# Kernel tuning notes

Measured on AMD Instinct MI355X. Metric: run time of the kernel, lower is better.

The kernel has to match this reference:

```python
import jax, jax.numpy as jnp
import numpy as np

H, B, F, D1, D21, D22, C = 10, 16384, 4, 2048, 2048, 2048, 2
OBS_X, OBS_Y, RADIUS = 40.0, 15.0, 6.0


def setup_inputs() -> dict:
    key = jax.random.key(0)
    ks = jax.random.split(key, 12)
    s = 0.02  # weight scale
    return {
        'x':   jax.random.normal(ks[0], (B, F), jnp.float32),
        'W1':  jax.random.normal(ks[1], (H, F, D1), jnp.float32) * s,
        'b1':  jnp.zeros((H, D1), jnp.float32),
        'W21': jax.random.normal(ks[2], (H, D1, D21), jnp.float32) * s,
        'b21': jnp.zeros((H, D21), jnp.float32),
        'W22': jax.random.normal(ks[3], (H, D1, D22), jnp.float32) * s,
        'b22': jnp.zeros((H, D22), jnp.float32),
        'W31': jax.random.normal(ks[4], (H, D21, C), jnp.float32) * s,
        'b31': jnp.zeros((H, C), jnp.float32),
        'W32': jax.random.normal(ks[5], (H, D22, C), jnp.float32) * s,
        'b32': jnp.zeros((H, C), jnp.float32),
        'wt':  jnp.ones((H,), jnp.float32),
        'mean': jax.random.normal(ks[6], (F,), jnp.float32),
        'std':  jnp.ones((F,), jnp.float32),
        'sgn': 1,
        'itr': 0,
    }


def reference(x, W1, b1, W21, b21, W22, b22, W31, b31, W32, b32, wt, mean, std, sgn, itr):
    # x: [B,F]; un-normalized state x0 = x*std + mean
    x0 = x * std + mean

    # --- 10-head small-MLP ensemble (batched over heads via einsum) ---
    h1  = jax.nn.relu(jnp.einsum('bf,hfd->hbd', x, W1) + b1[:, None, :])      # [H,B,D1]
    x21 = jax.nn.relu(jnp.einsum('hbd,hde->hbe', h1, W21) + b21[:, None, :])  # [H,B,D21]
    x22 = jax.nn.relu(jnp.einsum('hbd,hde->hbe', h1, W22) + b22[:, None, :])  # [H,B,D22]
    x31 = jnp.einsum('hbe,hec->hbc', x21, W31) + b31[:, None, :]              # [H,B,C] nominal control
    x32 = 4.0 * jax.nn.sigmoid(jnp.einsum('hbe,hec->hbc', x22, W32) + b32[:, None, :])  # [H,B,C] CBF params

    # --- dCBF constraint (shared across heads; depends only on x0) ---
    px, py, theta, v = x0[:, 0], x0[:, 1], x0[:, 2], x0[:, 3]
    dx, dy = px - OBS_X, py - OBS_Y
    st, ct = jnp.sin(theta), jnp.cos(theta)
    barrier = dx * dx + dy * dy - RADIUS * RADIUS                 # [B]
    barrier_dot = 2.0 * dx * v * ct + 2.0 * dy * v * st          # [B]
    Lf2b = 2.0 * v * v                                            # [B]
    LgLfbu1 = -2.0 * dx * v * st + 2.0 * dy * v * ct
    LgLfbu2 = 2.0 * dx * ct + 2.0 * dy * st
    G = jnp.stack([-LgLfbu1, -LgLfbu2], axis=-1)                  # [B,C]

    # sgn == 1 -> same branch for every head (i==0 or sgn==1)
    h_rhs = Lf2b + (x32[..., 0] + x32[..., 1]) * barrier_dot + x32[..., 0] * x32[..., 1] * barrier  # [H,B]

    # --- batched QP: min 0.5 u'u - x31'u  s.t. G u <= h  (Q = I) ---
    # closed-form single-constraint active set: u = x31 - relu(G.x31 - h)/||G||^2 * G
    Gu = jnp.einsum('bc,hbc->hb', G, x31)                         # [H,B]
    GG = jnp.sum(G * G, axis=-1)                                  # [B]
    lam = jax.nn.relu(Gu - h_rhs) / GG                            # [H,B]
    u = x31 - lam[..., None] * G[None, :, :]                      # [H,B,C]

    # --- softmax-weighted ensemble sum ---
    w = jax.nn.softmax(wt)                                        # [H]
    return jnp.einsum('h,hbc->bc', w, u)                          # [B,C]
```

## Files before the change

kernel.cpp:

```cpp
#include <hip/hip_runtime.h>
#include <hip/hip_bf16.h>
#include <stdint.h>

#define H_  10
#define B_  16384
#define F_  4
#define D_  2048
#define C_  2

typedef __attribute__((ext_vector_type(8)))  short  short8;
typedef __attribute__((ext_vector_type(16))) float  floatx16;

typedef const uint32_t __attribute__((address_space(1))) gu32;
typedef uint32_t       __attribute__((address_space(3))) lu32;

__device__ __forceinline__ void async16(const void* g, void* l) {
    __builtin_amdgcn_global_load_lds((gu32*)g, (lu32*)l, 16, 0, 0);
}

__device__ __forceinline__ short8 bc8(uint4 v) { return __builtin_bit_cast(short8, v); }

__device__ __forceinline__ uint32_t packbf(float a, float b) {
    a = fmaxf(a, 0.f); b = fmaxf(b, 0.f);
    const uint32_t ax = __builtin_bit_cast(uint32_t, a) + 0x8000u;
    const uint32_t bx = __builtin_bit_cast(uint32_t, b) + 0x8000u;
    return (ax >> 16) | (bx & 0xFFFF0000u);
}

__device__ __forceinline__ uint32_t f2bf(float f) {
    union { float f; uint32_t u; } a; a.f = f;
    uint32_t u = a.u;
    u += 0x7FFF + ((u >> 16) & 1);
    return u >> 16;
}
__device__ __forceinline__ uint32_t pack2bf(float a, float b) {
    return f2bf(a) | (f2bf(b) << 16);
}


__global__ __launch_bounds__(256) void k_convert(
    const float* __restrict__ W21, const float* __restrict__ W22,
    uint16_t* __restrict__ Bc)
{
    __shared__ float tile[64][65];
    const int z = blockIdx.z;
    const int h = z % H_;
    const float* src = (z < H_ ? W21 : W22) + (size_t)h * D_ * D_;
    uint16_t*   dst  = Bc + (size_t)h * 2 * D_ * D_ + (z < H_ ? 0 : (size_t)D_ * D_);
    const int k0 = blockIdx.x * 64, n0 = blockIdx.y * 64;
    const int t = threadIdx.x;

    const int c4 = (t & 15) * 4;
    const int rb = (t >> 4) * 4;
#pragma unroll
    for (int i = 0; i < 4; i++) {
        const float4 v = *(const float4*)(src + (size_t)(k0 + rb + i) * D_ + n0 + c4);
        tile[rb + i][c4 + 0] = v.x; tile[rb + i][c4 + 1] = v.y;
        tile[rb + i][c4 + 2] = v.z; tile[rb + i][c4 + 3] = v.w;
    }
    __syncthreads();
    const int n = t >> 2;
    const int cb = (t & 3) * 2;
#pragma unroll
    for (int j = 0; j < 2; j++) {
        const int kk = (cb + j) * 8;
        uint32_t pk[4];
#pragma unroll
        for (int e = 0; e < 4; e++)
            pk[e] = pack2bf(tile[kk + 2 * e][n], tile[kk + 2 * e + 1][n]);
        *(uint4*)(dst + (size_t)(n0 + n) * D_ + k0 + kk) = make_uint4(pk[0], pk[1], pk[2], pk[3]);
    }
}

__global__ __launch_bounds__(256) void k_zero(uint4* p, int n4) {
    const int i = blockIdx.x * 256 + threadIdx.x;
    if (i < n4) p[i] = make_uint4(0u, 0u, 0u, 0u);
}

__global__ __launch_bounds__(256) void k_h1(
    const float* __restrict__ x, const float* __restrict__ W1,
    const float* __restrict__ b1, uint16_t* __restrict__ h1t, int h)
{
    const int t = threadIdx.x;
    const int kc = t & 127;
    const int rh = t >> 7;
    const int k0 = kc * 16;
    const float* W1h = W1 + (size_t)h * F_ * D_;
    float w[4][16], bb[16];
#pragma unroll
    for (int f = 0; f < 4; f++)
#pragma unroll
        for (int j = 0; j < 16; j += 4) {
            const float4 v = *(const float4*)(W1h + f * D_ + k0 + j);
            w[f][j] = v.x; w[f][j+1] = v.y; w[f][j+2] = v.z; w[f][j+3] = v.w;
        }
#pragma unroll
    for (int j = 0; j < 16; j += 4) {
        const float4 v = *(const float4*)(b1 + (size_t)h * D_ + k0 + j);
        bb[j] = v.x; bb[j+1] = v.y; bb[j+2] = v.z; bb[j+3] = v.w;
    }
    const int rowBase = blockIdx.x * 16 + rh * 8;
#pragma unroll
    for (int rr = 0; rr < 8; rr++) {
        const int row = rowBase + rr;
        const float4 xv = *(const float4*)(x + (size_t)row * 4);
        uint32_t pk[8];
#pragma unroll
        for (int j = 0; j < 16; j += 2) {
            float aa = fmaf(xv.x, w[0][j], bb[j]);
            aa = fmaf(xv.y, w[1][j], aa);
            aa = fmaf(xv.z, w[2][j], aa);
            aa = fmaf(xv.w, w[3][j], aa);
            float bv = fmaf(xv.x, w[0][j+1], bb[j+1]);
            bv = fmaf(xv.y, w[1][j+1], bv);
            bv = fmaf(xv.z, w[2][j+1], bv);
            bv = fmaf(xv.w, w[3][j+1], bv);
            pk[j >> 1] = packbf(aa, bv);
        }
        uint16_t* d = h1t + (size_t)row * D_ + k0;
        *(uint4*)d       = make_uint4(pk[0], pk[1], pk[2], pk[3]);
        *(uint4*)(d + 8) = make_uint4(pk[4], pk[5], pk[6], pk[7]);
    }
}

__global__ __launch_bounds__(256, 4) void k_gemm(
    const uint16_t* __restrict__ h1t, const uint16_t* __restrict__ Bcw,
    const float* __restrict__ b21, const float* __restrict__ b22,
    const float* __restrict__ W31, const float* __restrict__ W32,
    float* __restrict__ acc31, float* __restrict__ acc32, int h)
{
    __shared__ uint4 smem[2048];

    const int bid = blockIdx.x;
    const int xcd = bid & 7, idx = bid >> 3;
    const int mt = xcd * 16 + (idx & 15), nt = idx >> 4;
    const int mBase = mt * 128, nBase = nt * 128;

    const int t = threadIdx.x;
    const int lane = t & 63, wid = t >> 6;
    const int l31 = lane & 31, hi = lane >> 5;
    const int wm = wid >> 1, wn = wid & 1;

    const uint16_t* Abase = h1t + (size_t)mBase * D_;
    const uint16_t* Bbase = Bcw + (size_t)h * (4096 * (size_t)D_) + (size_t)nBase * D_;
    int soff[4];
#pragma unroll
    for (int j = 0; j < 4; j++) {
        const int unit = j * 256 + t;
        const int row = unit >> 3;
        const int cc = (unit & 7) ^ (row & 7) ^ ((row >> 3) & 3);
        soff[j] = row * D_ + cc * 8;
    }
    const int wbase = wid * 64;

    floatx16 acc[2][2];
#pragma unroll
    for (int mi = 0; mi < 2; mi++)
#pragma unroll
        for (int nj = 0; nj < 2; nj++)
#pragma unroll
            for (int e = 0; e < 16; e++) acc[mi][nj][e] = 0.f;

    const int x7 = l31 & 7, s3 = l31 >> 3;

    for (int kt = 0; kt < D_; kt += 64) {
#pragma unroll
        for (int j = 0; j < 4; j++)
            async16(Abase + soff[j] + kt, smem + j * 256 + wbase);
#pragma unroll
        for (int j = 0; j < 4; j++)
            async16(Bbase + soff[j] + kt, smem + 1024 + j * 256 + wbase);
        asm volatile("s_waitcnt vmcnt(0)" ::: "memory");
        __builtin_amdgcn_sched_barrier(0);
        __builtin_amdgcn_s_barrier();

        __builtin_amdgcn_s_setprio(1);
#pragma unroll
        for (int kk = 0; kk < 4; kk++) {
            const int u7 = (kk * 2 + hi) ^ x7 ^ s3;
            short8 af[2], bf[2];
#pragma unroll
            for (int mi = 0; mi < 2; mi++)
                af[mi] = bc8(smem[(wm * 64 + mi * 32 + l31) * 8 + u7]);
#pragma unroll
            for (int nj = 0; nj < 2; nj++)
                bf[nj] = bc8(smem[1024 + (wn * 64 + nj * 32 + l31) * 8 + u7]);
#pragma unroll
            for (int mi = 0; mi < 2; mi++)
#pragma unroll
                for (int nj = 0; nj < 2; nj++)
                    acc[mi][nj] = __builtin_amdgcn_mfma_f32_32x32x16_bf16(
                        af[mi], bf[nj], acc[mi][nj], 0, 0, 0);
        }
        __builtin_amdgcn_s_setprio(0);
        __syncthreads();
    }

    const int p    = nBase >> 11;
    const int nloc = nBase & 2047;
    const float* b2p = (p ? b22 : b21) + (size_t)h * D_;
    const float* W3p = (p ? W32 : W31) + (size_t)h * D_ * C_;
    float* ab2 = (p ? acc32 : acc31) + (size_t)h * B_ * C_;

    float bs[2], w3x[2], w3y[2];
#pragma unroll
    for (int nj = 0; nj < 2; nj++) {
        const int e = nloc + wn * 64 + nj * 32 + l31;
        bs[nj] = b2p[e];
        const float2 w2 = *(const float2*)(W3p + e * 2);
        w3x[nj] = w2.x; w3y[nj] = w2.y;
    }
#pragma unroll
    for (int mi = 0; mi < 2; mi++)
#pragma unroll
        for (int r = 0; r < 16; r++) {
            const float v0 = fmaxf(acc[mi][0][r] + bs[0], 0.f);
            const float v1 = fmaxf(acc[mi][1][r] + bs[1], 0.f);
            float s0 = fmaf(v0, w3x[0], v1 * w3x[1]);
            float s1 = fmaf(v0, w3y[0], v1 * w3y[1]);
#pragma unroll
            for (int off = 1; off < 32; off <<= 1) {
                s0 += __shfl_xor(s0, off, 64);
                s1 += __shfl_xor(s1, off, 64);
            }
            if (l31 == 0) {
                const int row = mBase + wm * 64 + mi * 32 + (r & 3) + 8 * (r >> 2) + 4 * hi;
                atomicAdd(&ab2[row * C_ + 0], s0);
                atomicAdd(&ab2[row * C_ + 1], s1);
            }
        }
}

__global__ __launch_bounds__(256) void k_final(
    const float* __restrict__ x,
    const float* __restrict__ acc31, const float* __restrict__ acc32,
    const float* __restrict__ b31, const float* __restrict__ b32,
    const float* __restrict__ wt, const float* __restrict__ mean,
    const float* __restrict__ stdv, float* __restrict__ out)
{
    const int b = blockIdx.x * 256 + threadIdx.x;
    const float4 xb = *(const float4*)(x + (size_t)b * 4);
    const float px = xb.x * stdv[0] + mean[0];
    const float py = xb.y * stdv[1] + mean[1];
    const float th = xb.z * stdv[2] + mean[2];
    const float v  = xb.w * stdv[3] + mean[3];
    const float dx = px - 40.0f, dy = py - 15.0f;
    const float st = sinf(th), ct = cosf(th);
    const float barrier = dx * dx + dy * dy - 36.0f;
    const float bdot = 2.f * dx * v * ct + 2.f * dy * v * st;
    const float Lf2b = 2.f * v * v;
    const float G0 = -(-2.f * dx * v * st + 2.f * dy * v * ct);
    const float G1 = -(2.f * dx * ct + 2.f * dy * st);
    const float GG = G0 * G0 + G1 * G1;

    float we[H_];
    float wmax = wt[0];
    for (int h = 1; h < H_; h++) wmax = fmaxf(wmax, wt[h]);
    float wsum = 0.f;
    for (int h = 0; h < H_; h++) { we[h] = expf(wt[h] - wmax); wsum += we[h]; }

    float o0 = 0.f, o1 = 0.f;
#pragma unroll
    for (int h = 0; h < H_; h++) {
        const size_t idx = ((size_t)h * B_ + b) * 2;
        const float x310 = acc31[idx]     + b31[h * 2];
        const float x311 = acc31[idx + 1] + b31[h * 2 + 1];
        const float z0 = acc32[idx]     + b32[h * 2];
        const float z1 = acc32[idx + 1] + b32[h * 2 + 1];
        const float x320 = 4.f / (1.f + expf(-z0));
        const float x321 = 4.f / (1.f + expf(-z1));
        const float hr = Lf2b + (x320 + x321) * bdot + x320 * x321 * barrier;
        const float Gu = G0 * x310 + G1 * x311;
        const float lam = fmaxf(Gu - hr, 0.f) / GG;
        o0 += we[h] * (x310 - lam * G0);
        o1 += we[h] * (x311 - lam * G1);
    }
    out[b * 2]     = o0 / wsum;
    out[b * 2 + 1] = o1 / wsum;
}

extern "C" void kernel_launch(void* const* d_in, const int* in_sizes, int n_in,
                              void* d_out, int out_size, void* d_ws, size_t ws_size,
                              hipStream_t stream)
{
    const float* x    = (const float*)d_in[0];
    const float* W1   = (const float*)d_in[1];
    const float* b1   = (const float*)d_in[2];
    const float* W21  = (const float*)d_in[3];
    const float* b21  = (const float*)d_in[4];
    const float* W22  = (const float*)d_in[5];
    const float* b22  = (const float*)d_in[6];
    const float* W31  = (const float*)d_in[7];
    const float* b31  = (const float*)d_in[8];
    const float* W32  = (const float*)d_in[9];
    const float* b32  = (const float*)d_in[10];
    const float* wt   = (const float*)d_in[11];
    const float* mean = (const float*)d_in[12];
    const float* stdv = (const float*)d_in[13];
    float* out = (float*)d_out;

    char* ws = (char*)d_ws;
    uint16_t* Bc   = (uint16_t*)(ws);
    float* acc31   = (float*)(ws + 167772160);
    float* acc32   = (float*)(ws + 169082880);
    uint16_t* h1t  = (uint16_t*)(ws + 170393600);

    k_convert<<<dim3(32, 32, 20), 256, 0, stream>>>(W21, W22, Bc);
    k_zero<<<dim3(640), 256, 0, stream>>>((uint4*)acc31, 163840);
    for (int h = 0; h < H_; ++h) {
        k_h1<<<dim3(1024), 256, 0, stream>>>(x, W1, b1, h1t, h);
        k_gemm<<<dim3(4096), 256, 0, stream>>>(h1t, Bc, b21, b22, W31, W32,
                                               acc31, acc32, h);
    }
    k_final<<<dim3(64), 256, 0, stream>>>(x, acc31, acc32, b31, b32, wt, mean, stdv, out);
}
```

Before: 3.631 ms.

## Enlarge GEMM tiles to 256x256 with 8 waves and double-buffered LDS prefetch

The per-head GEMM moves from 128x128 tiles with 4 waves to 256x256 tiles with 8 waves, using 128 KB of dynamic LDS. The K loop becomes double-buffered: the next 64-wide K slice is loaded asynchronously while MFMAs run on the current one. Barriers split the LDS reads and MFMA bursts into phases. The aim is to cut global and L2 traffic per FLOP and hide load latency behind compute. The cost is one block per CU, more accumulator registers, more barriers, and fewer blocks per launch, which can leave some CUs idle.

```diff
diff --git a/kernel.cpp b/kernel.cpp
--- a/kernel.cpp
+++ b/kernel.cpp
@@ -123,77 +123,165 @@
     }
 }
 
-__global__ __launch_bounds__(256, 4) void k_gemm(
+__global__ __launch_bounds__(512, 2) void k_gemm(
     const uint16_t* __restrict__ h1t, const uint16_t* __restrict__ Bcw,
     const float* __restrict__ b21, const float* __restrict__ b22,
     const float* __restrict__ W31, const float* __restrict__ W32,
     float* __restrict__ acc31, float* __restrict__ acc32, int h)
 {
-    __shared__ uint4 smem[2048];
+    extern __shared__ uint4 smem[];
 
     const int bid = blockIdx.x;
     const int xcd = bid & 7, idx = bid >> 3;
-    const int mt = xcd * 16 + (idx & 15), nt = idx >> 4;
-    const int mBase = mt * 128, nBase = nt * 128;
+    const int mt = xcd * 8 + (idx & 7), nt = idx >> 3;
+    const int mBase = mt * 256, nBase = nt * 256;
 
     const int t = threadIdx.x;
     const int lane = t & 63, wid = t >> 6;
     const int l31 = lane & 31, hi = lane >> 5;
-    const int wm = wid >> 1, wn = wid & 1;
+    const int wm = wid >> 2, wn = wid & 3;
 
     const uint16_t* Abase = h1t + (size_t)mBase * D_;
     const uint16_t* Bbase = Bcw + (size_t)h * (4096 * (size_t)D_) + (size_t)nBase * D_;
     int soff[4];
 #pragma unroll
     for (int j = 0; j < 4; j++) {
-        const int unit = j * 256 + t;
+        const int unit = j * 512 + t;
         const int row = unit >> 3;
         const int cc = (unit & 7) ^ (row & 7) ^ ((row >> 3) & 3);
         soff[j] = row * D_ + cc * 8;
     }
-    const int wbase = wid * 64;
-
-    floatx16 acc[2][2];
-#pragma unroll
-    for (int mi = 0; mi < 2; mi++)
+
+    auto stageTile = [&](int buf, int kt) {
+#pragma unroll
+        for (int j = 0; j < 4; j++)
+            async16(Abase + soff[j] + kt, smem + buf * 4096 + j * 512 + t);
+#pragma unroll
+        for (int j = 0; j < 4; j++)
+            async16(Bbase + soff[j] + kt, smem + buf * 4096 + 2048 + j * 512 + t);
+    };
+
+    floatx16 acc[4][2];
+#pragma unroll
+    for (int mi = 0; mi < 4; mi++)
 #pragma unroll
         for (int nj = 0; nj < 2; nj++)
 #pragma unroll
             for (int e = 0; e < 16; e++) acc[mi][nj][e] = 0.f;
 
     const int x7 = l31 & 7, s3 = l31 >> 3;
-
-    for (int kt = 0; kt < D_; kt += 64) {
-#pragma unroll
-        for (int j = 0; j < 4; j++)
-            async16(Abase + soff[j] + kt, smem + j * 256 + wbase);
-#pragma unroll
-        for (int j = 0; j < 4; j++)
-            async16(Bbase + soff[j] + kt, smem + 1024 + j * 256 + wbase);
+    const int arow = wm * 128 + l31;
+    const int brow = wn * 64 + l31;
+
+    short8 a[2][2], b[2][2];
+
+    stageTile(0, 0);
+    asm volatile("s_waitcnt vmcnt(0)" ::: "memory");
+    __builtin_amdgcn_sched_barrier(0);
+    __builtin_amdgcn_s_barrier();
+
+#pragma unroll 1
+    for (int tt = 0; tt < 32; ++tt) {
+        const int buf = tt & 1;
+        const uint4* Ab = smem + buf * 4096;
+        const uint4* Bb = smem + buf * 4096 + 2048;
+
+        if (tt < 31) stageTile(buf ^ 1, (tt + 1) * 64);
+#pragma unroll
+        for (int kp = 0; kp < 2; kp++) {
+            const int u7 = (kp * 2 + hi) ^ x7 ^ s3;
+#pragma unroll
+            for (int i = 0; i < 2; i++)
+                a[i][kp] = bc8(Ab[(arow + i * 32) * 8 + u7]);
+#pragma unroll
+            for (int nj = 0; nj < 2; nj++)
+                b[nj][kp] = bc8(Bb[(brow + nj * 32) * 8 + u7]);
+        }
+        __builtin_amdgcn_s_barrier();
+        asm volatile("s_waitcnt lgkmcnt(0)" ::: "memory");
+        __builtin_amdgcn_sched_barrier(0);
+        __builtin_amdgcn_s_setprio(1);
+#pragma unroll
+        for (int kp = 0; kp < 2; kp++)
+#pragma unroll
+            for (int i = 0; i < 2; i++)
+#pragma unroll
+                for (int nj = 0; nj < 2; nj++)
+                    acc[i][nj] = __builtin_amdgcn_mfma_f32_32x32x16_bf16(
+                        a[i][kp], b[nj][kp], acc[i][nj], 0, 0, 0);
+        __builtin_amdgcn_s_setprio(0);
+        __builtin_amdgcn_s_barrier();
+
+#pragma unroll
+        for (int kp = 0; kp < 2; kp++) {
+            const int u7 = (kp * 2 + hi) ^ x7 ^ s3;
+#pragma unroll
+            for (int i = 0; i < 2; i++)
+                a[i][kp] = bc8(Ab[(arow + (i + 2) * 32) * 8 + u7]);
+        }
+        __builtin_amdgcn_s_barrier();
+        asm volatile("s_waitcnt lgkmcnt(0)" ::: "memory");
+        __builtin_amdgcn_sched_barrier(0);
+        __builtin_amdgcn_s_setprio(1);
+#pragma unroll
+        for (int kp = 0; kp < 2; kp++)
+#pragma unroll
+            for (int i = 0; i < 2; i++)
+#pragma unroll
+                for (int nj = 0; nj < 2; nj++)
+                    acc[i + 2][nj] = __builtin_amdgcn_mfma_f32_32x32x16_bf16(
+                        a[i][kp], b[nj][kp], acc[i + 2][nj], 0, 0, 0);
+        __builtin_amdgcn_s_setprio(0);
+        __builtin_amdgcn_s_barrier();
+
+#pragma unroll
+        for (int kp = 0; kp < 2; kp++) {
+            const int u7 = ((kp + 2) * 2 + hi) ^ x7 ^ s3;
+#pragma unroll
+            for (int i = 0; i < 2; i++)
+                a[i][kp] = bc8(Ab[(arow + i * 32) * 8 + u7]);
+#pragma unroll
+            for (int nj = 0; nj < 2; nj++)
+                b[nj][kp] = bc8(Bb[(brow + nj * 32) * 8 + u7]);
+        }
+        __builtin_amdgcn_s_barrier();
+        asm volatile("s_waitcnt lgkmcnt(0)" ::: "memory");
+        __builtin_amdgcn_sched_barrier(0);
+        __builtin_amdgcn_s_setprio(1);
+#pragma unroll
+        for (int kp = 0; kp < 2; kp++)
+#pragma unroll
+            for (int i = 0; i < 2; i++)
+#pragma unroll
+                for (int nj = 0; nj < 2; nj++)
+                    acc[i][nj] = __builtin_amdgcn_mfma_f32_32x32x16_bf16(
+                        a[i][kp], b[nj][kp], acc[i][nj], 0, 0, 0);
+        __builtin_amdgcn_s_setprio(0);
+        __builtin_amdgcn_s_barrier();
+
+#pragma unroll
+        for (int kp = 0; kp < 2; kp++) {
+            const int u7 = ((kp + 2) * 2 + hi) ^ x7 ^ s3;
+#pragma unroll
+            for (int i = 0; i < 2; i++)
+                a[i][kp] = bc8(Ab[(arow + (i + 2) * 32) * 8 + u7]);
+        }
+        __builtin_amdgcn_s_barrier();
+        asm volatile("s_waitcnt lgkmcnt(0)" ::: "memory");
+        __builtin_amdgcn_sched_barrier(0);
+        __builtin_amdgcn_s_setprio(1);
+#pragma unroll
+        for (int kp = 0; kp < 2; kp++)
+#pragma unroll
+            for (int i = 0; i < 2; i++)
+#pragma unroll
+                for (int nj = 0; nj < 2; nj++)
+                    acc[i + 2][nj] = __builtin_amdgcn_mfma_f32_32x32x16_bf16(
+                        a[i][kp], b[nj][kp], acc[i + 2][nj], 0, 0, 0);
+        __builtin_amdgcn_s_setprio(0);
         asm volatile("s_waitcnt vmcnt(0)" ::: "memory");
         __builtin_amdgcn_sched_barrier(0);
         __builtin_amdgcn_s_barrier();
-
-        __builtin_amdgcn_s_setprio(1);
-#pragma unroll
-        for (int kk = 0; kk < 4; kk++) {
-            const int u7 = (kk * 2 + hi) ^ x7 ^ s3;
-            short8 af[2], bf[2];
-#pragma unroll
-            for (int mi = 0; mi < 2; mi++)
-                af[mi] = bc8(smem[(wm * 64 + mi * 32 + l31) * 8 + u7]);
-#pragma unroll
-            for (int nj = 0; nj < 2; nj++)
-                bf[nj] = bc8(smem[1024 + (wn * 64 + nj * 32 + l31) * 8 + u7]);
-#pragma unroll
-            for (int mi = 0; mi < 2; mi++)
-#pragma unroll
-                for (int nj = 0; nj < 2; nj++)
-                    acc[mi][nj] = __builtin_amdgcn_mfma_f32_32x32x16_bf16(
-                        af[mi], bf[nj], acc[mi][nj], 0, 0, 0);
-        }
-        __builtin_amdgcn_s_setprio(0);
-        __syncthreads();
     }
 
     const int p    = nBase >> 11;
@@ -211,7 +299,7 @@
         w3x[nj] = w2.x; w3y[nj] = w2.y;
     }
 #pragma unroll
-    for (int mi = 0; mi < 2; mi++)
+    for (int mi = 0; mi < 4; mi++)
 #pragma unroll
         for (int r = 0; r < 16; r++) {
             const float v0 = fmaxf(acc[mi][0][r] + bs[0], 0.f);
@@ -224,7 +312,7 @@
                 s1 += __shfl_xor(s1, off, 64);
             }
             if (l31 == 0) {
-                const int row = mBase + wm * 64 + mi * 32 + (r & 3) + 8 * (r >> 2) + 4 * hi;
+                const int row = mBase + wm * 128 + mi * 32 + (r & 3) + 8 * (r >> 2) + 4 * hi;
                 atomicAdd(&ab2[row * C_ + 0], s0);
                 atomicAdd(&ab2[row * C_ + 1], s1);
             }
@@ -305,12 +393,19 @@
     float* acc32   = (float*)(ws + 169082880);
     uint16_t* h1t  = (uint16_t*)(ws + 170393600);
 
+    static bool attr_done = false;
+    if (!attr_done) {
+        hipFuncSetAttribute(reinterpret_cast<const void*>(k_gemm),
+                            hipFuncAttributeMaxDynamicSharedMemorySize, 131072);
+        attr_done = true;
+    }
+
     k_convert<<<dim3(32, 32, 20), 256, 0, stream>>>(W21, W22, Bc);
     k_zero<<<dim3(640), 256, 0, stream>>>((uint4*)acc31, 163840);
     for (int h = 0; h < H_; ++h) {
         k_h1<<<dim3(1024), 256, 0, stream>>>(x, W1, b1, h1t, h);
-        k_gemm<<<dim3(4096), 256, 0, stream>>>(h1t, Bc, b21, b22, W31, W32,
-                                               acc31, acc32, h);
+        k_gemm<<<dim3(1024), 512, 131072, stream>>>(h1t, Bc, b21, b22, W31, W32,
+                                                    acc31, acc32, h);
     }
     k_final<<<dim3(64), 256, 0, stream>>>(x, acc31, acc32, b31, b32, wt, mean, stdv, out);
 }
```

Result: slower. 4.190 ms (+15.4%).
